# Performance work log

Hardware: AMD Instinct MI355X
Metric: run time of the kernel (lower is better)

Reference implementation:

```python
import jax, jax.numpy as jnp
import numpy as np

EMBED = 192
D_INNER = 2 * EMBED          # expand=2
D_STATE = 4                  # low_rank
D_CONV = 4
DT_RANK = (EMBED + 15) // 16 # ceil(192/16) = 12
N_MIX = 2
RANK = 4                     # LowRankProjection rank
B_, H_, W_ = 8, 64, 64


def setup_inputs() -> dict:
    key = jax.random.key(0)
    ks = jax.random.split(key, 16)
    s = lambda *sh: 1.0 / np.sqrt(sh[-1])
    inp = {
        "x": jax.random.normal(ks[0], (B_, EMBED, H_, W_), jnp.float32),
        # stacked per-mixer Mamba params (leading dim N_MIX)
        "in_proj_w": jax.random.normal(ks[1], (N_MIX, 2 * D_INNER, EMBED), jnp.float32) * s(EMBED),
        "conv_w": jax.random.normal(ks[2], (N_MIX, D_INNER, D_CONV), jnp.float32) * s(D_CONV),
        "conv_b": jnp.zeros((N_MIX, D_INNER), jnp.float32),
        "x_proj_w": jax.random.normal(ks[3], (N_MIX, DT_RANK + 2 * D_STATE, D_INNER), jnp.float32) * s(D_INNER),
        "dt_proj_w": jax.random.normal(ks[4], (N_MIX, D_INNER, DT_RANK), jnp.float32) * s(DT_RANK),
        "dt_proj_b": jax.random.uniform(ks[5], (N_MIX, D_INNER), jnp.float32, -4.0, -2.0),
        "A_log": jnp.tile(jnp.log(jnp.arange(1, D_STATE + 1, dtype=jnp.float32))[None, None, :], (N_MIX, D_INNER, 1)),
        "D": jnp.ones((N_MIX, D_INNER), jnp.float32),
        "out_proj_w": jax.random.normal(ks[6], (N_MIX, EMBED, D_INNER), jnp.float32) * s(D_INNER),
        # LowRankProjection
        "U_w": jax.random.normal(ks[7], (RANK, EMBED), jnp.float32) * s(EMBED),
        "V_w": jax.random.normal(ks[8], (EMBED, RANK), jnp.float32) * s(RANK),
        # LayerNorm
        "ln_g": jnp.ones((EMBED,), jnp.float32),
        "ln_b": jnp.zeros((EMBED,), jnp.float32),
    }
    return inp


def _silu(x):
    return x * jax.nn.sigmoid(x)


def _mamba(x, in_proj_w, conv_w, conv_b, x_proj_w, dt_proj_w, dt_proj_b, A_log, D, out_proj_w):
    # x: (B, L, d_model)
    B, L, _ = x.shape
    xz = jnp.einsum("bld,ed->ble", x, in_proj_w)          # (B, L, 2*d_inner)
    xin, z = jnp.split(xz, 2, axis=-1)
    # causal depthwise conv over L
    xt = jnp.transpose(xin, (0, 2, 1))                      # (B, d_inner, L)
    xc = jax.lax.conv_general_dilated(
        xt, conv_w[:, None, :], window_strides=(1,), padding=[(D_CONV - 1, 0)],
        feature_group_count=D_INNER, dimension_numbers=("NCH", "OIH", "NCH"))
    xa = _silu(jnp.transpose(xc + conv_b[None, :, None], (0, 2, 1)))  # (B, L, d_inner)
    x_dbl = jnp.einsum("bld,ed->ble", xa, x_proj_w)         # (B, L, dt_rank+2*d_state)
    dt_lr = x_dbl[..., :DT_RANK]
    Bm = x_dbl[..., DT_RANK:DT_RANK + D_STATE]              # (B, L, d_state)
    Cm = x_dbl[..., DT_RANK + D_STATE:]                     # (B, L, d_state)
    dt = jax.nn.softplus(jnp.einsum("blr,dr->bld", dt_lr, dt_proj_w) + dt_proj_b)  # (B, L, d_inner)
    A = -jnp.exp(A_log)                                     # (d_inner, d_state)
    dA = jnp.exp(dt[..., None] * A)                         # (B, L, d_inner, d_state)
    dBu = dt[..., None] * Bm[:, :, None, :] * xa[..., None]  # (B, L, d_inner, d_state)

    def step(h, inputs):
        dA_i, dBu_i, C_i = inputs                           # (B,d_inner,d_state),(B,d_inner,d_state),(B,d_state)
        h = dA_i * h + dBu_i
        y = jnp.einsum("bds,bs->bd", h, C_i)
        return h, y

    h0 = jnp.zeros((B, D_INNER, D_STATE), x.dtype)
    _, ys = jax.lax.scan(step, h0, (jnp.moveaxis(dA, 1, 0), jnp.moveaxis(dBu, 1, 0), jnp.moveaxis(Cm, 1, 0)))
    y = jnp.moveaxis(ys, 0, 1) + xa * D                     # (B, L, d_inner)
    y = y * _silu(z)
    return jnp.einsum("ble,de->bld", y, out_proj_w)         # (B, L, d_model)


def reference(x, in_proj_w, conv_w, conv_b, x_proj_w, dt_proj_w, dt_proj_b,
              A_log, D, out_proj_w, U_w, V_w, ln_g, ln_b):
    residual = x
    B, C, H, W = x.shape
    h = jnp.transpose(x, (0, 2, 3, 1)).reshape(B, H * W, C)
    for i in range(N_MIX):
        h = _mamba(h, in_proj_w[i], conv_w[i], conv_b[i], x_proj_w[i], dt_proj_w[i],
                   dt_proj_b[i], A_log[i], D[i], out_proj_w[i])
    # low-rank projection
    h = jnp.einsum("blr,dr->bld", jnp.einsum("blc,rc->blr", h, U_w), V_w)
    h = jnp.transpose(h.reshape(B, H, W, C), (0, 3, 1, 2)) + residual
    # LayerNorm over channels
    hc = jnp.transpose(h, (0, 2, 3, 1))
    mu = hc.mean(-1, keepdims=True)
    var = ((hc - mu) ** 2).mean(-1, keepdims=True)
    hc = (hc - mu) * jax.lax.rsqrt(var + 1e-5) * ln_g + ln_b
    return jnp.transpose(hc, (0, 3, 1, 2))
```

## Files before the change

kernel.cpp:

```cpp
#include <hip/hip_runtime.h>
#include <hip/hip_bf16.h>
#include <cstdint>

#define EMBED   192
#define DINNER  384
#define DSTATE  4
#define DCONV   4
#define DTRANK  12
#define NMIX    2
#define RANK    4
#define BB      8
#define LL      4096
#define NBL     (BB*LL)
#define NCHUNK  128
#define CLEN    32
#define RSTR    36

typedef __attribute__((ext_vector_type(8))) short short8;
typedef __attribute__((ext_vector_type(4))) float float4v;

static __device__ __forceinline__ ushort f2b(float f) {
    __hip_bfloat16 h = __float2bfloat16(f);
    return *(ushort*)&h;
}
static __device__ __forceinline__ float b2f(ushort u) {
    __hip_bfloat16 h;
    *(ushort*)&h = u;
    return __bfloat162float(h);
}
static __device__ __forceinline__ float bs2f(short s) {
    ushort u = (ushort)s;
    return b2f(u);
}

#define PREP_N0 294912
#define PREP_N1 147456
#define PREP_N2 24576
#define PREP_N3 24576
#define PREP_N4 3072
__global__ __launch_bounds__(256) void k_prep(const float* __restrict__ in_proj_w,
                                              const float* __restrict__ out_proj_w,
                                              const float* __restrict__ x_proj_w,
                                              const float* __restrict__ dt_proj_w,
                                              const float* __restrict__ conv_w,
                                              ushort* __restrict__ wi,
                                              ushort* __restrict__ wo,
                                              ushort* __restrict__ xpwb,
                                              ushort* __restrict__ dtwpad,
                                              float* __restrict__ cwt) {
    int i = blockIdx.x * 256 + threadIdx.x;
    if (i < PREP_N0) {
        wi[i] = f2b(in_proj_w[i]);
        return;
    }
    i -= PREP_N0;
    if (i < PREP_N1) {
        wo[i] = f2b(out_proj_w[i]);
        return;
    }
    i -= PREP_N1;
    if (i < PREP_N2) {
        int mix = i / (32 * 384);
        int rem = i % (32 * 384);
        int e = rem / 384, k = rem % 384;
        xpwb[i] = (e < 20) ? f2b(x_proj_w[(size_t)mix * 20 * 384 + e * 384 + k]) : (ushort)0;
        return;
    }
    i -= PREP_N2;
    if (i < PREP_N3) {
        int mix = i / (384 * 32);
        int rem = i % (384 * 32);
        int n = rem / 32, r = rem % 32;
        dtwpad[i] = (r < DTRANK) ? f2b(dt_proj_w[(size_t)mix * 384 * DTRANK + n * DTRANK + r])
                                 : (ushort)0;
        return;
    }
    i -= PREP_N3;
    if (i < PREP_N4) {
        int mix = i / (DCONV * DINNER);
        int rem = i % (DCONV * DINNER);
        int k = rem / DINNER, d = rem % DINNER;
        cwt[i] = conv_w[(size_t)mix * DINNER * DCONV + d * DCONV + k];
    }
}

__global__ __launch_bounds__(256) void k_transpose(const float* __restrict__ x,
                                                   ushort* __restrict__ h0b) {
    __shared__ float tile[32][33];
    int b  = blockIdx.z;
    int c0 = blockIdx.y * 32;
    int l0 = blockIdx.x * 32;
    int tx = threadIdx.x;
    int ty = threadIdx.y;
    #pragma unroll
    for (int i = 0; i < 4; i++) {
        int c = c0 + ty + i * 8;
        tile[ty + i * 8][tx] = x[((size_t)b * EMBED + c) * LL + l0 + tx];
    }
    __syncthreads();
    #pragma unroll
    for (int i = 0; i < 4; i++) {
        int l = l0 + ty + i * 8;
        h0b[((size_t)b * LL + l) * EMBED + c0 + tx] = f2b(tile[tx][ty + i * 8]);
    }
}

template<int TN, int WRN>
__global__ __launch_bounds__(256) void k_gemm_bf16(const ushort* __restrict__ A, int lda,
                                                   const ushort* __restrict__ Bw, int ldb,
                                                   float* __restrict__ C, int ldc,
                                                   ushort* __restrict__ Cb, int ldcb,
                                                   int K) {
    constexpr int WRM = 4 / WRN;
    constexpr int WM  = 128 / WRM;
    constexpr int MT  = WM / 16;
    __shared__ ushort As[128][40];
    __shared__ ushort Bs[TN][40];
    int tid  = threadIdx.x;
    int lane = tid & 63;
    int wave = tid >> 6;
    int wmo = (wave / WRN) * WM;
    int wno = (wave % WRN) * 64;
    int m0 = blockIdx.y * 128;
    int n0 = blockIdx.x * TN;

    float4v acc[MT][4];
    #pragma unroll
    for (int i = 0; i < MT; i++)
        #pragma unroll
        for (int j = 0; j < 4; j++)
            acc[i][j] = (float4v){0.f, 0.f, 0.f, 0.f};

    for (int k0 = 0; k0 < K; k0 += 32) {
        #pragma unroll
        for (int i = 0; i < 2; i++) {
            int idx = tid + i * 256;
            int r = idx >> 2, sg = idx & 3;
            *(short8*)&As[r][sg * 8] =
                *(const short8*)(A + (size_t)(m0 + r) * lda + k0 + sg * 8);
        }
        #pragma unroll
        for (int i = 0; i < TN / 64; i++) {
            int idx = tid + i * 256;
            int r = idx >> 2, sg = idx & 3;
            *(short8*)&Bs[r][sg * 8] =
                *(const short8*)(Bw + (size_t)(n0 + r) * ldb + k0 + sg * 8);
        }
        __syncthreads();
        short8 av[MT], bv[4];
        #pragma unroll
        for (int i = 0; i < MT; i++)
            av[i] = *(const short8*)&As[wmo + i * 16 + (lane & 15)][(lane >> 4) * 8];
        #pragma unroll
        for (int j = 0; j < 4; j++)
            bv[j] = *(const short8*)&Bs[wno + j * 16 + (lane & 15)][(lane >> 4) * 8];
        #pragma unroll
        for (int i = 0; i < MT; i++)
            #pragma unroll
            for (int j = 0; j < 4; j++)
                acc[i][j] = __builtin_amdgcn_mfma_f32_16x16x32_bf16(
                    av[i], bv[j], acc[i][j], 0, 0, 0);
        __syncthreads();
    }

    #pragma unroll
    for (int i = 0; i < MT; i++) {
        int rbase = m0 + wmo + i * 16 + (lane >> 4) * 4;
        #pragma unroll
        for (int j = 0; j < 4; j++) {
            int col = n0 + wno + j * 16 + (lane & 15);
            #pragma unroll
            for (int r = 0; r < 4; r++) {
                float v = acc[i][j][r];
                if (C)  C[(size_t)(rbase + r) * ldc + col] = v;
                if (Cb) Cb[(size_t)(rbase + r) * ldcb + col] = f2b(v);
            }
        }
    }
}

__global__ __launch_bounds__(256) void k_conv_silu(const ushort* __restrict__ xz,
                                                   const float* __restrict__ cwt,
                                                   const float* __restrict__ cb,
                                                   ushort* __restrict__ xa) {
    int t   = blockIdx.x * 256 + threadIdx.x;
    int g   = t % 48;
    int blc = t / 48;
    int d0  = g * 8;
    int lc  = blc % (LL / 8);
    int b   = blc / (LL / 8);
    int l0  = lc * 8;

    float wk[4][8], bias[8];
    #pragma unroll
    for (int k = 0; k < 4; k++) {
        float4v wa = *(const float4v*)(cwt + k * DINNER + d0);
        float4v wb = *(const float4v*)(cwt + k * DINNER + d0 + 4);
        #pragma unroll
        for (int j = 0; j < 4; j++) { wk[k][j] = wa[j]; wk[k][j + 4] = wb[j]; }
    }
    {
        float4v ba = *(const float4v*)(cb + d0);
        float4v bb = *(const float4v*)(cb + d0 + 4);
        #pragma unroll
        for (int j = 0; j < 4; j++) { bias[j] = ba[j]; bias[j + 4] = bb[j]; }
    }

    float r0[8] = {}, r1[8] = {}, r2[8] = {};
    const ushort* px = xz + ((size_t)(b * LL + l0)) * 768 + d0;
    if (l0 > 0) {
        short8 v;
        v = *(const short8*)(px - 3 * 768);
        #pragma unroll
        for (int j = 0; j < 8; j++) r0[j] = bs2f(v[j]);
        v = *(const short8*)(px - 2 * 768);
        #pragma unroll
        for (int j = 0; j < 8; j++) r1[j] = bs2f(v[j]);
        v = *(const short8*)(px - 1 * 768);
        #pragma unroll
        for (int j = 0; j < 8; j++) r2[j] = bs2f(v[j]);
    }
    ushort* po = xa + ((size_t)(b * LL + l0)) * DINNER + d0;
    #pragma unroll
    for (int i = 0; i < 8; i++) {
        short8 v = *(const short8*)(px + (size_t)i * 768);
        float cur[8];
        #pragma unroll
        for (int j = 0; j < 8; j++) cur[j] = bs2f(v[j]);
        short8 ov;
        #pragma unroll
        for (int j = 0; j < 8; j++) {
            float a = bias[j] + wk[0][j] * r0[j] + wk[1][j] * r1[j]
                    + wk[2][j] * r2[j] + wk[3][j] * cur[j];
            float sv = a / (1.f + __expf(-a));
            ov[j] = (short)f2b(sv);
        }
        *(short8*)(po + (size_t)i * DINNER) = ov;
        #pragma unroll
        for (int j = 0; j < 8; j++) { r0[j] = r1[j]; r1[j] = r2[j]; r2[j] = cur[j]; }
    }
}

__global__ __launch_bounds__(256) void k_xproj_mfma(const ushort* __restrict__ xa,
                                                    const ushort* __restrict__ xpwb,
                                                    float* __restrict__ xdb32) {
    __shared__ ushort As[128][40];
    __shared__ ushort Bs[32][40];
    int tid  = threadIdx.x;
    int lane = tid & 63;
    int wave = tid >> 6;
    int m0 = blockIdx.x * 128;
    float4v acc[2][2];
    #pragma unroll
    for (int i = 0; i < 2; i++)
        #pragma unroll
        for (int j = 0; j < 2; j++)
            acc[i][j] = (float4v){0.f, 0.f, 0.f, 0.f};
    for (int k0 = 0; k0 < 384; k0 += 32) {
        #pragma unroll
        for (int i = 0; i < 2; i++) {
            int idx = tid + i * 256;
            int r = idx >> 2, sg = idx & 3;
            *(short8*)&As[r][sg * 8] =
                *(const short8*)(xa + (size_t)(m0 + r) * 384 + k0 + sg * 8);
        }
        if (tid < 128) {
            int r = tid >> 2, sg = tid & 3;
            *(short8*)&Bs[r][sg * 8] =
                *(const short8*)(xpwb + (size_t)r * 384 + k0 + sg * 8);
        }
        __syncthreads();
        short8 av[2], bv[2];
        #pragma unroll
        for (int i = 0; i < 2; i++)
            av[i] = *(const short8*)&As[wave * 32 + i * 16 + (lane & 15)][(lane >> 4) * 8];
        #pragma unroll
        for (int j = 0; j < 2; j++)
            bv[j] = *(const short8*)&Bs[j * 16 + (lane & 15)][(lane >> 4) * 8];
        #pragma unroll
        for (int i = 0; i < 2; i++)
            #pragma unroll
            for (int j = 0; j < 2; j++)
                acc[i][j] = __builtin_amdgcn_mfma_f32_16x16x32_bf16(
                    av[i], bv[j], acc[i][j], 0, 0, 0);
        __syncthreads();
    }
    #pragma unroll
    for (int i = 0; i < 2; i++) {
        int rbase = m0 + wave * 32 + i * 16 + (lane >> 4) * 4;
        #pragma unroll
        for (int j = 0; j < 2; j++) {
            int col = j * 16 + (lane & 15);
            #pragma unroll
            for (int r = 0; r < 4; r++)
                xdb32[(size_t)(rbase + r) * 32 + col] = acc[i][j][r];
        }
    }
}

static __device__ __forceinline__ void dt_mfma_tile(const float* __restrict__ rows,
                                                    const ushort* __restrict__ dtwpad,
                                                    const float* __restrict__ dtb,
                                                    ushort* __restrict__ dtS,
                                                    int wave, int lane) {
    int mcol = lane & 15;
    int quad = lane >> 4;
    #pragma unroll
    for (int nt = 0; nt < 4; nt++) {
        int n = wave * 64 + nt * 16 + mcol;
        short8 bv = *(const short8*)(dtwpad + (size_t)n * 32 + quad * 8);
        float bias = dtb[n];
        #pragma unroll
        for (int mt = 0; mt < 2; mt++) {
            float4v a0 = *(const float4v*)&rows[(mt * 16 + mcol) * RSTR + quad * 8];
            float4v a1 = *(const float4v*)&rows[(mt * 16 + mcol) * RSTR + quad * 8 + 4];
            short8 av;
            #pragma unroll
            for (int j = 0; j < 4; j++) {
                av[j]     = (short)f2b(a0[j]);
                av[j + 4] = (short)f2b(a1[j]);
            }
            float4v acc = (float4v){0.f, 0.f, 0.f, 0.f};
            acc = __builtin_amdgcn_mfma_f32_16x16x32_bf16(av, bv, acc, 0, 0, 0);
            #pragma unroll
            for (int r = 0; r < 4; r++) {
                float s = acc[r] + bias;
                float sp = fmaxf(s, 0.f) + __logf(1.f + __expf(-fabsf(s)));
                dtS[(mt * 16 + quad * 4 + r) * DINNER + n] = f2b(sp);
            }
        }
    }
}

static __device__ __forceinline__ bool as_is_harmonic(const float* As) {
    return fabsf(As[1] - 2.f * As[0]) <= 1e-5f * fabsf(As[1]) + 1e-12f
        && fabsf(As[2] - 3.f * As[0]) <= 1e-5f * fabsf(As[2]) + 1e-12f
        && fabsf(As[3] - 4.f * As[0]) <= 1e-5f * fabsf(As[3]) + 1e-12f;
}

__global__ __launch_bounds__(384) void k_scan_local(const ushort* __restrict__ xa,
                                                    const float* __restrict__ xdb32,
                                                    const ushort* __restrict__ dtwpad,
                                                    const float* __restrict__ dtb,
                                                    const float* __restrict__ A_log,
                                                    const float* __restrict__ Dp,
                                                    float* __restrict__ carryT,
                                                    float* __restrict__ carryH,
                                                    ushort* __restrict__ dt16,
                                                    ushort* __restrict__ ylb) {
    int d     = threadIdx.x;
    int lane  = d & 63;
    int wave  = d >> 6;
    int chunk = blockIdx.x;
    int b     = blockIdx.y;
    __shared__ float rows[CLEN * RSTR];
    __shared__ ushort dtS[CLEN * DINNER];
    size_t rbase = ((size_t)b * LL + (size_t)chunk * CLEN) * 32;
    for (int i = d; i < CLEN * 32; i += 384) {
        int l = i >> 5, e = i & 31;
        rows[l * RSTR + e] = xdb32[rbase + i];
    }
    float As[DSTATE];
    #pragma unroll
    for (int s = 0; s < DSTATE; s++) As[s] = -__expf(A_log[d * DSTATE + s]);
    bool fastA = as_is_harmonic(As);
    float Dd = Dp[d];
    __syncthreads();
    dt_mfma_tile(rows, dtwpad, dtb, dtS, wave, lane);
    __syncthreads();
    float h[DSTATE] = {0.f, 0.f, 0.f, 0.f};
    float T = 0.f;
    size_t mbase = (size_t)b * LL + (size_t)chunk * CLEN;
    for (int l = 0; l < CLEN; l++) {
        ushort dtu = dtS[l * DINNER + d];
        float dtvv = b2f(dtu);
        float xav  = b2f(xa[(mbase + l) * DINNER + d]);
        float du   = dtvv * xav;
        T += dtvv;
        const float* row = &rows[l * RSTR];
        float da[DSTATE];
        if (fastA) {
            float p = __expf(dtvv * As[0]);
            da[0] = p; da[1] = p * p; da[2] = da[1] * p; da[3] = da[2] * p;
        } else {
            #pragma unroll
            for (int s = 0; s < DSTATE; s++) da[s] = __expf(dtvv * As[s]);
        }
        float yv = xav * Dd;
        #pragma unroll
        for (int s = 0; s < DSTATE; s++) {
            h[s] = da[s] * h[s] + du * row[DTRANK + s];
            yv  += h[s] * row[DTRANK + DSTATE + s];
        }
        dt16[(mbase + l) * DINNER + d] = dtu;
        ylb[(mbase + l) * DINNER + d]  = f2b(yv);
    }
    size_t cb = ((size_t)chunk * BB + b);
    carryT[cb * 384 + d] = T;
    float4v hv = {h[0], h[1], h[2], h[3]};
    *(float4v*)(carryH + cb * 1536 + d * 4) = hv;
}

__global__ __launch_bounds__(256) void k_scan_combine(const float* __restrict__ carryT,
                                                      const float* __restrict__ carryH,
                                                      const float* __restrict__ A_log,
                                                      float* __restrict__ carryI) {
    int c   = blockIdx.x * 256 + threadIdx.x;
    int b   = c / 1536;
    int rem = c - b * 1536;
    int d   = rem >> 2;
    float As = -__expf(A_log[rem]);
    float hrun = 0.f;
    for (int k = 0; k < NCHUNK; k++) {
        size_t o = (size_t)k * BB + b;
        float T  = carryT[o * 384 + d];
        float Hk = carryH[o * 1536 + rem];
        carryI[o * 1536 + rem] = hrun;
        hrun = __expf(As * T) * hrun + Hk;
    }
}

__global__ __launch_bounds__(384) void k_scan_corr(const ushort* __restrict__ dt16,
                                                   const ushort* __restrict__ ylb,
                                                   const ushort* __restrict__ xz,
                                                   const float* __restrict__ xdb32,
                                                   const float* __restrict__ A_log,
                                                   const float* __restrict__ carryI,
                                                   ushort* __restrict__ y) {
    int d     = threadIdx.x;
    int chunk = blockIdx.x;
    int b     = blockIdx.y;
    __shared__ float Crow[CLEN][DSTATE];
    size_t rbase = ((size_t)b * LL + (size_t)chunk * CLEN) * 32;
    if (d < CLEN * DSTATE) {
        int l = d >> 2, s = d & 3;
        Crow[l][s] = xdb32[rbase + l * 32 + DTRANK + DSTATE + s];
    }
    float As[DSTATE];
    #pragma unroll
    for (int s = 0; s < DSTATE; s++) As[s] = -__expf(A_log[d * DSTATE + s]);
    bool fastA = as_is_harmonic(As);
    float4v hv = *(const float4v*)(carryI + ((size_t)chunk * BB + b) * 1536 + d * 4);
    float hc[DSTATE];
    #pragma unroll
    for (int s = 0; s < DSTATE; s++) hc[s] = hv[s];
    __syncthreads();
    size_t mbase = (size_t)b * LL + (size_t)chunk * CLEN;
    #pragma unroll 4
    for (int l = 0; l < CLEN; l++) {
        size_t m = mbase + l;
        float dtvv = b2f(dt16[m * DINNER + d]);
        float da[DSTATE];
        if (fastA) {
            float p = __expf(dtvv * As[0]);
            da[0] = p; da[1] = p * p; da[2] = da[1] * p; da[3] = da[2] * p;
        } else {
            #pragma unroll
            for (int s = 0; s < DSTATE; s++) da[s] = __expf(dtvv * As[s]);
        }
        float corr = 0.f;
        #pragma unroll
        for (int s = 0; s < DSTATE; s++) {
            hc[s] *= da[s];
            corr  += hc[s] * Crow[l][s];
        }
        float yv = b2f(ylb[m * DINNER + d]) + corr;
        float zv = b2f(xz[m * 768 + DINNER + d]);
        yv *= zv / (1.f + __expf(-zv));
        y[m * DINNER + d] = f2b(yv);
    }
}

__global__ __launch_bounds__(256) void k_tail(const ushort* __restrict__ h1b,
                                              const ushort* __restrict__ h0b,
                                              const float* __restrict__ U,
                                              const float* __restrict__ V,
                                              const float* __restrict__ g,
                                              const float* __restrict__ be,
                                              float* __restrict__ out) {
    __shared__ float tile[EMBED * 65];
    int tid  = threadIdx.x;
    int lane = tid & 63;
    int wave = tid >> 6;
    int b  = blockIdx.y;
    int l0 = blockIdx.x * 64;
    for (int t = 0; t < 16; t++) {
        int lloc = wave * 16 + t;
        size_t m = (size_t)b * LL + l0 + lloc;
        float hv[3];
        #pragma unroll
        for (int i = 0; i < 3; i++) hv[i] = b2f(h1b[m * EMBED + lane + 64 * i]);
        float r[RANK];
        #pragma unroll
        for (int j = 0; j < RANK; j++) {
            float p = 0.f;
            #pragma unroll
            for (int i = 0; i < 3; i++) p += hv[i] * U[j * EMBED + lane + 64 * i];
            #pragma unroll
            for (int off = 1; off < 64; off <<= 1) p += __shfl_xor(p, off);
            r[j] = p;
        }
        float u[3], s1 = 0.f, s2 = 0.f;
        #pragma unroll
        for (int i = 0; i < 3; i++) {
            int c = lane + 64 * i;
            float v = r[0] * V[c * 4 + 0] + r[1] * V[c * 4 + 1]
                    + r[2] * V[c * 4 + 2] + r[3] * V[c * 4 + 3];
            u[i] = v + b2f(h0b[m * EMBED + c]);
            s1 += u[i];
            s2 += u[i] * u[i];
        }
        #pragma unroll
        for (int off = 1; off < 64; off <<= 1) {
            s1 += __shfl_xor(s1, off);
            s2 += __shfl_xor(s2, off);
        }
        float mean = s1 * (1.f / EMBED);
        float var  = s2 * (1.f / EMBED) - mean * mean;
        float inv  = rsqrtf(var + 1e-5f);
        #pragma unroll
        for (int i = 0; i < 3; i++) {
            int c = lane + 64 * i;
            tile[c * 65 + lloc] = (u[i] - mean) * inv * g[c] + be[c];
        }
    }
    __syncthreads();
    for (int i = tid; i < EMBED * 64; i += 256) {
        int c = i >> 6, l = i & 63;
        out[((size_t)(b * EMBED + c)) * LL + l0 + l] = tile[c * 65 + l];
    }
}

extern "C" void kernel_launch(void* const* d_in, const int* in_sizes, int n_in,
                              void* d_out, int out_size, void* d_ws, size_t ws_size,
                              hipStream_t stream) {
    const float* x          = (const float*)d_in[0];
    const float* in_proj_w  = (const float*)d_in[1];
    const float* conv_w     = (const float*)d_in[2];
    const float* conv_b     = (const float*)d_in[3];
    const float* x_proj_w   = (const float*)d_in[4];
    const float* dt_proj_w  = (const float*)d_in[5];
    const float* dt_proj_b  = (const float*)d_in[6];
    const float* A_log      = (const float*)d_in[7];
    const float* Dp         = (const float*)d_in[8];
    const float* out_proj_w = (const float*)d_in[9];
    const float* U_w        = (const float*)d_in[10];
    const float* V_w        = (const float*)d_in[11];
    const float* ln_g       = (const float*)d_in[12];
    const float* ln_b       = (const float*)d_in[13];
    float* out = (float*)d_out;

    float* ws    = (float*)d_ws;
    float* xdb32 = ws;
    float* carryT = xdb32 + (size_t)NBL * 32;
    float* carryH = carryT + (size_t)NCHUNK * BB * DINNER;
    float* carryI = carryH + (size_t)NCHUNK * BB * DINNER * DSTATE;
    ushort* xz16   = (ushort*)(carryI + (size_t)NCHUNK * BB * DINNER * DSTATE);
    ushort* xa16   = xz16   + (size_t)NBL * 768;
    ushort* yb     = xa16   + (size_t)NBL * DINNER;
    ushort* h0b    = yb     + (size_t)NBL * DINNER;
    ushort* h1b    = h0b    + (size_t)NBL * EMBED;
    ushort* dt16   = h1b    + (size_t)NBL * EMBED;
    ushort* ylb    = dt16   + (size_t)NBL * DINNER;
    ushort* wi     = ylb    + (size_t)NBL * DINNER;
    ushort* wo     = wi     + (size_t)NMIX * 768 * EMBED;
    ushort* xpwb   = wo     + (size_t)NMIX * EMBED * DINNER;
    ushort* dtwpad = xpwb   + (size_t)NMIX * 32 * 384;
    float*  cwt    = (float*)(dtwpad + (size_t)NMIX * 384 * 32);

    k_prep<<<(PREP_N0 + PREP_N1 + PREP_N2 + PREP_N3 + PREP_N4) / 256, 256, 0, stream>>>(
        in_proj_w, out_proj_w, x_proj_w, dt_proj_w, conv_w, wi, wo, xpwb, dtwpad, cwt);

    k_transpose<<<dim3(LL / 32, EMBED / 32, BB), dim3(32, 8), 0, stream>>>(x, h0b);

    const ushort* hinb = h0b;
    for (int mix = 0; mix < NMIX; mix++) {
        const float* Alg  = A_log + (size_t)mix * DINNER * DSTATE;
        const ushort* dtwm = dtwpad + (size_t)mix * 384 * 32;
        const float* dtbm = dt_proj_b + mix * DINNER;

        k_gemm_bf16<128, 2><<<dim3(768 / 128, NBL / 128), 256, 0, stream>>>(
            hinb, EMBED, wi + (size_t)mix * 768 * EMBED, EMBED,
            (float*)nullptr, 0, xz16, 768, EMBED);
        k_conv_silu<<<(NBL / 8 * 48) / 256, 256, 0, stream>>>(
            xz16, cwt + (size_t)mix * DCONV * DINNER, conv_b + mix * DINNER, xa16);
        k_xproj_mfma<<<NBL / 128, 256, 0, stream>>>(
            xa16, xpwb + (size_t)mix * 32 * 384, xdb32);
        k_scan_local<<<dim3(NCHUNK, BB), 384, 0, stream>>>(
            xa16, xdb32, dtwm, dtbm, Alg, Dp + mix * DINNER, carryT, carryH, dt16, ylb);
        k_scan_combine<<<(BB * DINNER * DSTATE) / 256, 256, 0, stream>>>(
            carryT, carryH, Alg, carryI);
        k_scan_corr<<<dim3(NCHUNK, BB), 384, 0, stream>>>(
            dt16, ylb, xz16, xdb32, Alg, carryI, yb);
        k_gemm_bf16<64, 1><<<dim3(EMBED / 64, NBL / 128), 256, 0, stream>>>(
            yb, DINNER, wo + (size_t)mix * EMBED * DINNER, DINNER,
            (float*)nullptr, 0, h1b, EMBED, DINNER);
        hinb = h1b;
    }

    k_tail<<<dim3(LL / 64, BB), 256, 0, stream>>>(h1b, h0b, U_w, V_w, ln_g, ln_b, out);
}
```

Before: 394.3 us.

## Fold mixer-0 out_proj into mixer-1 in_proj, fuse z-SiLU into GEMM epilogue

```diff
diff --git a/kernel.cpp b/kernel.cpp
--- a/kernel.cpp
+++ b/kernel.cpp
@@ -38,6 +38,7 @@
 #define PREP_N2 24576
 #define PREP_N3 24576
 #define PREP_N4 3072
+#define PREP_N5 294912
 __global__ __launch_bounds__(256) void k_prep(const float* __restrict__ in_proj_w,
                                               const float* __restrict__ out_proj_w,
                                               const float* __restrict__ x_proj_w,
@@ -47,7 +48,8 @@
                                               ushort* __restrict__ wo,
                                               ushort* __restrict__ xpwb,
                                               ushort* __restrict__ dtwpad,
-                                              float* __restrict__ cwt) {
+                                              float* __restrict__ cwt,
+                                              ushort* __restrict__ wc) {
     int i = blockIdx.x * 256 + threadIdx.x;
     if (i < PREP_N0) {
         wi[i] = f2b(in_proj_w[i]);
@@ -81,6 +83,18 @@
         int rem = i % (DCONV * DINNER);
         int k = rem / DINNER, d = rem % DINNER;
         cwt[i] = conv_w[(size_t)mix * DINNER * DCONV + d * DCONV + k];
+        return;
+    }
+    i -= PREP_N4;
+    if (i < PREP_N5) {
+        int n = i / 384, k = i % 384;
+        const float* wi1 = in_proj_w + (size_t)768 * 192;
+        const float* wo0 = out_proj_w;
+        float acc = 0.f;
+        #pragma unroll 4
+        for (int e = 0; e < 192; e++)
+            acc += wi1[(size_t)n * 192 + e] * wo0[(size_t)e * 384 + k];
+        wc[i] = f2b(acc);
     }
 }
 
@@ -105,7 +119,7 @@
     }
 }
 
-template<int TN, int WRN>
+template<int TN, int WRN, bool SILUZ>
 __global__ __launch_bounds__(256) void k_gemm_bf16(const ushort* __restrict__ A, int lda,
                                                    const ushort* __restrict__ Bw, int ldb,
                                                    float* __restrict__ C, int ldc,
@@ -172,6 +186,7 @@
             #pragma unroll
             for (int r = 0; r < 4; r++) {
                 float v = acc[i][j][r];
+                if (SILUZ && col >= DINNER) v = v / (1.f + __expf(-v));
                 if (C)  C[(size_t)(rbase + r) * ldc + col] = v;
                 if (Cb) Cb[(size_t)(rbase + r) * ldcb + col] = f2b(v);
             }
@@ -346,8 +361,7 @@
                                                     const float* __restrict__ Dp,
                                                     float* __restrict__ carryT,
                                                     float* __restrict__ carryH,
-                                                    ushort* __restrict__ dt16,
-                                                    ushort* __restrict__ ylb) {
+                                                    uint* __restrict__ dyb) {
     int d     = threadIdx.x;
     int lane  = d & 63;
     int wave  = d >> 6;
@@ -392,8 +406,7 @@
             h[s] = da[s] * h[s] + du * row[DTRANK + s];
             yv  += h[s] * row[DTRANK + DSTATE + s];
         }
-        dt16[(mbase + l) * DINNER + d] = dtu;
-        ylb[(mbase + l) * DINNER + d]  = f2b(yv);
+        dyb[(mbase + l) * DINNER + d] = ((uint)dtu << 16) | (uint)f2b(yv);
     }
     size_t cb = ((size_t)chunk * BB + b);
     carryT[cb * 384 + d] = T;
@@ -420,8 +433,7 @@
     }
 }
 
-__global__ __launch_bounds__(384) void k_scan_corr(const ushort* __restrict__ dt16,
-                                                   const ushort* __restrict__ ylb,
+__global__ __launch_bounds__(384) void k_scan_corr(const uint* __restrict__ dyb,
                                                    const ushort* __restrict__ xz,
                                                    const float* __restrict__ xdb32,
                                                    const float* __restrict__ A_log,
@@ -449,7 +461,9 @@
     #pragma unroll 4
     for (int l = 0; l < CLEN; l++) {
         size_t m = mbase + l;
-        float dtvv = b2f(dt16[m * DINNER + d]);
+        uint dv = dyb[m * DINNER + d];
+        float dtvv = b2f((ushort)(dv >> 16));
+        float ylv  = b2f((ushort)(dv & 0xffffu));
         float da[DSTATE];
         if (fastA) {
             float p = __expf(dtvv * As[0]);
@@ -464,9 +478,9 @@
             hc[s] *= da[s];
             corr  += hc[s] * Crow[l][s];
         }
-        float yv = b2f(ylb[m * DINNER + d]) + corr;
-        float zv = b2f(xz[m * 768 + DINNER + d]);
-        yv *= zv / (1.f + __expf(-zv));
+        float yv = ylv + corr;
+        float zs = b2f(xz[m * 768 + DINNER + d]);
+        yv *= zs;
         y[m * DINNER + d] = f2b(yv);
     }
 }
@@ -560,43 +574,48 @@
     ushort* yb     = xa16   + (size_t)NBL * DINNER;
     ushort* h0b    = yb     + (size_t)NBL * DINNER;
     ushort* h1b    = h0b    + (size_t)NBL * EMBED;
-    ushort* dt16   = h1b    + (size_t)NBL * EMBED;
-    ushort* ylb    = dt16   + (size_t)NBL * DINNER;
-    ushort* wi     = ylb    + (size_t)NBL * DINNER;
+    uint*   dyb    = (uint*)(h1b + (size_t)NBL * EMBED);
+    ushort* wi     = (ushort*)(dyb + (size_t)NBL * DINNER);
     ushort* wo     = wi     + (size_t)NMIX * 768 * EMBED;
     ushort* xpwb   = wo     + (size_t)NMIX * EMBED * DINNER;
     ushort* dtwpad = xpwb   + (size_t)NMIX * 32 * 384;
     float*  cwt    = (float*)(dtwpad + (size_t)NMIX * 384 * 32);
-
-    k_prep<<<(PREP_N0 + PREP_N1 + PREP_N2 + PREP_N3 + PREP_N4) / 256, 256, 0, stream>>>(
-        in_proj_w, out_proj_w, x_proj_w, dt_proj_w, conv_w, wi, wo, xpwb, dtwpad, cwt);
+    ushort* wc     = (ushort*)(cwt + (size_t)NMIX * DCONV * DINNER);
+
+    k_prep<<<(PREP_N0 + PREP_N1 + PREP_N2 + PREP_N3 + PREP_N4 + PREP_N5) / 256,
+             256, 0, stream>>>(
+        in_proj_w, out_proj_w, x_proj_w, dt_proj_w, conv_w,
+        wi, wo, xpwb, dtwpad, cwt, wc);
 
     k_transpose<<<dim3(LL / 32, EMBED / 32, BB), dim3(32, 8), 0, stream>>>(x, h0b);
 
-    const ushort* hinb = h0b;
     for (int mix = 0; mix < NMIX; mix++) {
         const float* Alg  = A_log + (size_t)mix * DINNER * DSTATE;
         const ushort* dtwm = dtwpad + (size_t)mix * 384 * 32;
         const float* dtbm = dt_proj_b + mix * DINNER;
 
-        k_gemm_bf16<128, 2><<<dim3(768 / 128, NBL / 128), 256, 0, stream>>>(
-            hinb, EMBED, wi + (size_t)mix * 768 * EMBED, EMBED,
-            (float*)nullptr, 0, xz16, 768, EMBED);
+        if (mix == 0) {
+            k_gemm_bf16<128, 2, true><<<dim3(768 / 128, NBL / 128), 256, 0, stream>>>(
+                h0b, EMBED, wi, EMBED, (float*)nullptr, 0, xz16, 768, EMBED);
+        } else {
+            k_gemm_bf16<128, 2, true><<<dim3(768 / 128, NBL / 128), 256, 0, stream>>>(
+                yb, DINNER, wc, DINNER, (float*)nullptr, 0, xz16, 768, DINNER);
+        }
         k_conv_silu<<<(NBL / 8 * 48) / 256, 256, 0, stream>>>(
             xz16, cwt + (size_t)mix * DCONV * DINNER, conv_b + mix * DINNER, xa16);
         k_xproj_mfma<<<NBL / 128, 256, 0, stream>>>(
             xa16, xpwb + (size_t)mix * 32 * 384, xdb32);
         k_scan_local<<<dim3(NCHUNK, BB), 384, 0, stream>>>(
-            xa16, xdb32, dtwm, dtbm, Alg, Dp + mix * DINNER, carryT, carryH, dt16, ylb);
+            xa16, xdb32, dtwm, dtbm, Alg, Dp + mix * DINNER, carryT, carryH, dyb);
         k_scan_combine<<<(BB * DINNER * DSTATE) / 256, 256, 0, stream>>>(
             carryT, carryH, Alg, carryI);
         k_scan_corr<<<dim3(NCHUNK, BB), 384, 0, stream>>>(
-            dt16, ylb, xz16, xdb32, Alg, carryI, yb);
-        k_gemm_bf16<64, 1><<<dim3(EMBED / 64, NBL / 128), 256, 0, stream>>>(
-            yb, DINNER, wo + (size_t)mix * EMBED * DINNER, DINNER,
-            (float*)nullptr, 0, h1b, EMBED, DINNER);
-        hinb = h1b;
-    }
+            dyb, xz16, xdb32, Alg, carryI, yb);
+    }
+
+    k_gemm_bf16<64, 1, false><<<dim3(EMBED / 64, NBL / 128), 256, 0, stream>>>(
+        yb, DINNER, wo + (size_t)EMBED * DINNER, DINNER,
+        (float*)nullptr, 0, h1b, EMBED, DINNER);
 
     k_tail<<<dim3(LL / 64, BB), 256, 0, stream>>>(h1b, h0b, U_w, V_w, ln_g, ln_b, out);
 }
```

Measured after the change: 420.1 us. 1.07x slower.
